# Performance work log

Measured on AMD Instinct MI355X. Metric: run time of the kernel, lower is better.

## Reference

```python
import jax, jax.numpy as jnp
import numpy as np

DT = 0.01
NJ = 7
GRAV = 9.81
Q_LOWER = jnp.array([-2.9671, -1.8326, -2.9671, -3.1416, -2.9671, -0.0873, -2.9671], jnp.float32)
Q_UPPER = jnp.array([ 2.9671,  1.8326,  2.9671,  0.0,     2.9671,  3.8223,  2.9671], jnp.float32)


def _skew(v):
    z = jnp.zeros((), v.dtype)
    return jnp.stack([jnp.stack([z, -v[2], v[1]]),
                      jnp.stack([v[2], z, -v[0]]),
                      jnp.stack([-v[1], v[0], z])])


def _mot_X(E, r):
    # 6x6 spatial motion transform [[E,0],[-E*skew(r),E]]
    zero = jnp.zeros_like(E)
    top = jnp.concatenate([E, zero], axis=1)
    bot = jnp.concatenate([-E @ _skew(r), E], axis=1)
    return jnp.concatenate([top, bot], axis=0)


def _crm(v):
    # spatial motion cross-product matrix for v=[w;v0]
    Sw, Sv = _skew(v[:3]), _skew(v[3:])
    zero = jnp.zeros_like(Sw)
    top = jnp.concatenate([Sw, zero], axis=1)
    bot = jnp.concatenate([Sv, Sw], axis=1)
    return jnp.concatenate([top, bot], axis=0)


def _step_single(x, u, axes, R_tree, p_tree, I_sp):
    dt_ = x.dtype
    q = jnp.clip(x[:NJ], Q_LOWER.astype(dt_), Q_UPPER.astype(dt_))
    qd = x[NJ:]
    # forward kinematics: per-joint 6x6 child<-parent transforms and motion subspaces
    Xups, Ss = [], []
    eye3 = jnp.eye(3, dtype=dt_)
    for i in range(NJ):
        a = axes[i]
        c, s = jnp.cos(q[i]), jnp.sin(q[i])
        R = c * eye3 + s * _skew(a) + (1.0 - c) * jnp.outer(a, a)  # rodrigues
        Xj = _mot_X(R.T, jnp.zeros(3, dt_))
        Xt = _mot_X(R_tree[i], p_tree[i])
        Xups.append(Xj @ Xt)
        Ss.append(jnp.concatenate([a, jnp.zeros(3, dt_)]))
    # RNEA bias force h (qdd=0, gravity, zero base velocity, identity base pose)
    v_prev = jnp.zeros(6, dt_)
    a_prev = jnp.array([0.0, 0.0, 0.0, 0.0, 0.0, GRAV], dt_)  # a_base = -g trick
    fs = []
    for i in range(NJ):
        vJ = Ss[i] * qd[i]
        v = Xups[i] @ v_prev + vJ
        acc = Xups[i] @ a_prev + _crm(v) @ vJ
        Iv = I_sp[i] @ v
        f = I_sp[i] @ acc - _crm(v).T @ Iv  # crf(v) = -crm(v)^T
        fs.append(f)
        v_prev, a_prev = v, acc
    h = [None] * NJ
    for i in range(NJ - 1, -1, -1):
        h[i] = Ss[i] @ fs[i]
        if i > 0:
            fs[i - 1] = fs[i - 1] + Xups[i].T @ fs[i]
    h = jnp.stack(h)
    # CRBA mass matrix (serial chain, parent(i)=i-1)
    Ic = [I_sp[i] for i in range(NJ)]
    M = jnp.zeros((NJ, NJ), dt_)
    for i in range(NJ - 1, -1, -1):
        if i > 0:
            Ic[i - 1] = Ic[i - 1] + Xups[i].T @ Ic[i] @ Xups[i]
        F = Ic[i] @ Ss[i]
        M = M.at[i, i].set(Ss[i] @ F)
        for j in range(i - 1, -1, -1):
            F = Xups[j + 1].T @ F
            mij = Ss[j] @ F
            M = M.at[i, j].set(mij).at[j, i].set(mij)
    M = M + 1e-8 * jnp.eye(NJ, dtype=dt_)
    qdd = jnp.linalg.solve(M, (u - h)[:, None])[:, 0]
    qd_new = qd + DT * qdd
    q_new = q + DT * qd_new
    return jnp.concatenate([q_new, qd_new])


def setup_inputs() -> dict:
    B = 65536
    key = jax.random.key(0)
    k1, k2 = jax.random.split(key)
    x = jax.random.normal(k1, (B, 14), jnp.float32)
    u = jax.random.normal(k2, (B, 7), jnp.float32)
    rng = np.random.default_rng(0)
    # unit joint axes
    axes = rng.normal(size=(NJ, 3))
    axes = axes / np.linalg.norm(axes, axis=1, keepdims=True)
    # orthonormal fixed parent->child rotations (det +1)
    R_tree = np.empty((NJ, 3, 3))
    for i in range(NJ):
        Q, _ = np.linalg.qr(rng.normal(size=(3, 3)))
        if np.linalg.det(Q) < 0:
            Q[:, 0] = -Q[:, 0]
        R_tree[i] = Q
    p_tree = 0.2 * rng.normal(size=(NJ, 3))
    # SPD 6x6 spatial inertias: [[Ibar, m*Cx],[m*Cx^T, m*I3]]
    I_sp = np.empty((NJ, 6, 6))
    for i in range(NJ):
        m = float(rng.uniform(1.0, 5.0))
        c = 0.05 * rng.normal(size=3)
        Cx = np.array([[0, -c[2], c[1]], [c[2], 0, -c[0]], [-c[1], c[0], 0]])
        A = 0.1 * rng.normal(size=(3, 3))
        Ic_ = A @ A.T + 0.05 * np.eye(3)
        Ibar = Ic_ + m * Cx @ Cx.T
        I_sp[i] = np.block([[Ibar, m * Cx], [m * Cx.T, m * np.eye(3)]])
    return {
        "x": x, "u": u,
        "axes": jnp.asarray(axes, jnp.float32),
        "R_tree": jnp.asarray(R_tree, jnp.float32),
        "p_tree": jnp.asarray(p_tree, jnp.float32),
        "I_sp": jnp.asarray(I_sp, jnp.float32),
    }


def reference(x, u, axes, R_tree, p_tree, I_sp):
    return jax.vmap(_step_single, in_axes=(0, 0, None, None, None, None))(
        x, u, axes, R_tree, p_tree, I_sp)
```

## Files before the change

kernel.cpp:

```cpp
#include <hip/hip_runtime.h>
#include <math.h>

#define NJ 7
#define DTF 0.01f
#define GRAVF 9.81f
#define MIX(i,j) ((i)*((i)+1)/2 + (j))
#define MPAD 29
#define FSTR 43
#define SNC  15
#define QST  9

__device__ __forceinline__ void cross3(const float* a, const float* b, float* o){
    o[0] = a[1]*b[2] - a[2]*b[1];
    o[1] = a[2]*b[0] - a[0]*b[2];
    o[2] = a[0]*b[1] - a[1]*b[0];
}
__device__ __forceinline__ void mv3(const float* E, const float* x, float* y){
    y[0] = E[0]*x[0] + E[1]*x[1] + E[2]*x[2];
    y[1] = E[3]*x[0] + E[4]*x[1] + E[5]*x[2];
    y[2] = E[6]*x[0] + E[7]*x[1] + E[8]*x[2];
}
__device__ __forceinline__ void mtv3(const float* E, const float* x, float* y){
    y[0] = E[0]*x[0] + E[3]*x[1] + E[6]*x[2];
    y[1] = E[1]*x[0] + E[4]*x[1] + E[7]*x[2];
    y[2] = E[2]*x[0] + E[5]*x[1] + E[8]*x[2];
}
__device__ __forceinline__ void symv(const float* S, const float* x, float* y){
    y[0] = S[0]*x[0] + S[1]*x[1] + S[2]*x[2];
    y[1] = S[1]*x[0] + S[3]*x[1] + S[4]*x[2];
    y[2] = S[2]*x[0] + S[4]*x[1] + S[5]*x[2];
}
__device__ __forceinline__ void mm3(const float* A, const float* B, float* o){
#pragma unroll
    for (int r = 0; r < 3; r++)
#pragma unroll
        for (int c = 0; c < 3; c++)
            o[r*3+c] = A[r*3]*B[c] + A[r*3+1]*B[3+c] + A[r*3+2]*B[6+c];
}
__device__ __forceinline__ void congr(const float* E, const float* X, float* o){
    float t[9];
#pragma unroll
    for (int r = 0; r < 3; r++)
#pragma unroll
        for (int c = 0; c < 3; c++)
            t[r*3+c] = E[r]*X[c] + E[3+r]*X[3+c] + E[6+r]*X[6+c];
    mm3(t, E, o);
}
__device__ __forceinline__ void makeE(const float* a, const float* __restrict__ Rt,
                                      float s, float c, float* E){
    float omc = 1.0f - c;
    float RT[9];
    RT[0] = c + omc*a[0]*a[0];       RT[1] =  s*a[2] + omc*a[0]*a[1]; RT[2] = -s*a[1] + omc*a[0]*a[2];
    RT[3] = -s*a[2] + omc*a[1]*a[0]; RT[4] = c + omc*a[1]*a[1];       RT[5] =  s*a[0] + omc*a[1]*a[2];
    RT[6] =  s*a[1] + omc*a[2]*a[0]; RT[7] = -s*a[0] + omc*a[2]*a[1]; RT[8] = c + omc*a[2]*a[2];
    float Rl[9];
#pragma unroll
    for (int k = 0; k < 9; k++) Rl[k] = Rt[k];
    mm3(RT, Rl, E);
}
__device__ __forceinline__ void bodyI(const float* __restrict__ g_I, int i,
                                      float* SA, float* h, float& m){
    const float* I6 = g_I + i*36;
    SA[0]=I6[0]; SA[1]=I6[1]; SA[2]=I6[2];
    SA[3]=I6[7]; SA[4]=I6[8]; SA[5]=I6[14];
    h[0]=I6[16]; h[1]=I6[5]; h[2]=I6[9];
    m = I6[21];
}

__constant__ float QL_c[NJ] = {-2.9671f,-1.8326f,-2.9671f,-3.1416f,-2.9671f,-0.0873f,-2.9671f};
__constant__ float QU_c[NJ] = { 2.9671f, 1.8326f, 2.9671f, 0.0f,    2.9671f, 3.8223f, 2.9671f};

__global__ __launch_bounds__(128)
void panda_step(const float* __restrict__ x, const float* __restrict__ u,
                const float* __restrict__ g_ax, const float* __restrict__ g_Rt,
                const float* __restrict__ g_pt, const float* __restrict__ g_I,
                float* __restrict__ out, int B)
{
    __shared__ float s_M[64*MPAD];
    __shared__ float s_F[2*64*FSTR];
    __shared__ float s_snc[64*SNC];
    __shared__ float s_qd[64*QST];
    __shared__ float s_rhs[64*QST];

    const int role = threadIdx.x >> 6;
    const int lane = threadIdx.x & 63;
    const int e    = blockIdx.x*64 + lane;
    const bool act = (e < B);

    float q[NJ], qd[NJ];
    if (act && role == 0){
        float xl[14];
        const float2* x2 = (const float2*)(x + e*14);
#pragma unroll
        for (int i = 0; i < 7; i++){ float2 v = x2[i]; xl[2*i] = v.x; xl[2*i+1] = v.y; }
#pragma unroll
        for (int i = 0; i < NJ; i++){
            q[i]  = fminf(fmaxf(xl[i], QL_c[i]), QU_c[i]);
            qd[i] = xl[NJ + i];
            float s, c; __sincosf(q[i], &s, &c);
            s_snc[lane*SNC + i]     = s;
            s_snc[lane*SNC + 7 + i] = c;
            s_qd[lane*QST + i]      = qd[i];
            s_rhs[lane*QST + i]     = u[e*NJ + i];
        }
    }
    __syncthreads();

    if (act && role == 1){
        float* Fb = &s_F[64*FSTR + lane*FSTR];
        float SA[6], hc[3], mc;
        bodyI(g_I, 6, SA, hc, mc);
#pragma unroll 1
        for (int i = NJ-1; i >= 0; --i){
            float a[3] = { g_ax[3*i], g_ax[3*i+1], g_ax[3*i+2] };
            float p[3] = { g_pt[3*i], g_pt[3*i+1], g_pt[3*i+2] };
            float Ft[3]; symv(SA, a, Ft);
            Fb[i*6+0]=Ft[0]; Fb[i*6+1]=Ft[1]; Fb[i*6+2]=Ft[2];
            Fb[i*6+3] = a[1]*hc[2] - a[2]*hc[1];
            Fb[i*6+4] = a[2]*hc[0] - a[0]*hc[2];
            Fb[i*6+5] = a[0]*hc[1] - a[1]*hc[0];
#pragma unroll 1
            for (int k = i; k < NJ; ++k){
                float f0=Fb[k*6], f1=Fb[k*6+1], f2=Fb[k*6+2];
                s_M[lane*MPAD + k*(k+1)/2 + i] = a[0]*f0 + a[1]*f1 + a[2]*f2;
            }
            if (i > 0){
                float snv = s_snc[lane*SNC+i], csv = s_snc[lane*SNC+7+i];
                float E[9]; makeE(a, g_Rt + 9*i, snv, csv, E);
                float SAm[6], hm[3], mm_;
                bodyI(g_I, i-1, SAm, hm, mm_);
                float Af[9] = {SA[0],SA[1],SA[2], SA[1],SA[3],SA[4], SA[2],SA[4],SA[5]};
                float Ap[9]; congr(E, Af, Ap);
                float hr[3]; mtv3(E, hc, hr);
                float hpd = hr[0]*p[0]+hr[1]*p[1]+hr[2]*p[2];
                float ppd = p[0]*p[0]+p[1]*p[1]+p[2]*p[2];
                float dga = 2.0f*hpd + mc*ppd;
                SA[0] = Ap[0] - 2.0f*p[0]*hr[0] - mc*p[0]*p[0] + dga + SAm[0];
                SA[1] = Ap[1] - p[0]*hr[1] - hr[0]*p[1] - mc*p[0]*p[1] + SAm[1];
                SA[2] = Ap[2] - p[0]*hr[2] - hr[0]*p[2] - mc*p[0]*p[2] + SAm[2];
                SA[3] = Ap[4] - 2.0f*p[1]*hr[1] - mc*p[1]*p[1] + dga + SAm[3];
                SA[4] = Ap[5] - p[1]*hr[2] - hr[1]*p[2] - mc*p[1]*p[2] + SAm[4];
                SA[5] = Ap[8] - 2.0f*p[2]*hr[2] - mc*p[2]*p[2] + dga + SAm[5];
                hc[0] = hr[0] + mc*p[0] + hm[0];
                hc[1] = hr[1] + mc*p[1] + hm[1];
                hc[2] = hr[2] + mc*p[2] + hm[2];
                mc += mm_;
#pragma unroll 1
                for (int k = i; k < NJ; ++k){
                    float ft[3] = {Fb[k*6+0], Fb[k*6+1], Fb[k*6+2]};
                    float fb[3] = {Fb[k*6+3], Fb[k*6+4], Fb[k*6+5]};
                    float tm[3], tf[3], cp[3];
                    mtv3(E, ft, tm); mtv3(E, fb, tf);
                    cross3(p, tf, cp);
                    Fb[k*6+0]=tm[0]+cp[0]; Fb[k*6+1]=tm[1]+cp[1]; Fb[k*6+2]=tm[2]+cp[2];
                    Fb[k*6+3]=tf[0];       Fb[k*6+4]=tf[1];       Fb[k*6+5]=tf[2];
                }
            }
        }
        float Mx[28];
#pragma unroll
        for (int j = 0; j < 28; j++) Mx[j] = s_M[lane*MPAD + j];
#pragma unroll
        for (int i = 0; i < NJ; i++) Mx[MIX(i,i)] += 1e-8f;
#pragma unroll
        for (int k = 0; k < NJ; k++){
            float d = Mx[MIX(k,k)];
#pragma unroll
            for (int j = 0; j < NJ; j++) if (j < k) d -= Mx[MIX(k,j)]*Mx[MIX(k,j)];
            float linv = __builtin_amdgcn_rsqf(d);
            Mx[MIX(k,k)] = linv;
#pragma unroll
            for (int i2 = k+1; i2 < NJ; i2++){
                float s2 = Mx[MIX(i2,k)];
#pragma unroll
                for (int j = 0; j < NJ; j++) if (j < k) s2 -= Mx[MIX(i2,j)]*Mx[MIX(k,j)];
                Mx[MIX(i2,k)] = s2 * linv;
            }
        }
#pragma unroll
        for (int j = 0; j < 28; j++) s_M[lane*MPAD + j] = Mx[j];
    }
    else if (act){
        float* Fb = &s_F[lane*FSTR];
        float w[3]  = {0.f,0.f,0.f}, vl[3] = {0.f,0.f,0.f};
        float aw[3] = {0.f,0.f,0.f}, av[3] = {0.f,0.f,GRAVF};
#pragma unroll 1
        for (int i = 0; i < NJ; ++i){
            float a[3] = { g_ax[3*i], g_ax[3*i+1], g_ax[3*i+2] };
            float p[3] = { g_pt[3*i], g_pt[3*i+1], g_pt[3*i+2] };
            float snv = s_snc[lane*SNC+i], csv = s_snc[lane*SNC+7+i];
            float qdi = s_qd[lane*QST+i];
            float E[9]; makeE(a, g_Rt + 9*i, snv, csv, E);
            float tw[3]; mv3(E, w, tw);
            float nw[3] = { tw[0]+a[0]*qdi, tw[1]+a[1]*qdi, tw[2]+a[2]*qdi };
            float cwp[3]; cross3(w, p, cwp);
            float t1[3] = { vl[0]+cwp[0], vl[1]+cwp[1], vl[2]+cwp[2] };
            float nvl[3]; mv3(E, t1, nvl);
            float taw[3]; mv3(E, aw, taw);
            float cna[3]; cross3(nw, a, cna);
            float naw[3] = { taw[0]+qdi*cna[0], taw[1]+qdi*cna[1], taw[2]+qdi*cna[2] };
            float cap[3]; cross3(aw, p, cap);
            float t2[3] = { av[0]+cap[0], av[1]+cap[1], av[2]+cap[2] };
            float tav[3]; mv3(E, t2, tav);
            float cva[3]; cross3(nvl, a, cva);
            float nav[3] = { tav[0]+qdi*cva[0], tav[1]+qdi*cva[1], tav[2]+qdi*cva[2] };
            float SAi[6], hi[3], mi; bodyI(g_I, i, SAi, hi, mi);
            float Ivt[3], Iat[3], hxv[3], hxa[3];
            symv(SAi, nw, Ivt);  cross3(hi, nvl, hxv);
            symv(SAi, naw, Iat); cross3(hi, nav, hxa);
#pragma unroll
            for (int k = 0; k < 3; k++){ Ivt[k] += hxv[k]; Iat[k] += hxa[k]; }
            float hxw[3], hxaw[3];
            cross3(hi, nw, hxw); cross3(hi, naw, hxaw);
            float Ivb[3] = { mi*nvl[0]-hxw[0], mi*nvl[1]-hxw[1], mi*nvl[2]-hxw[2] };
            float Iab[3] = { mi*nav[0]-hxaw[0], mi*nav[1]-hxaw[1], mi*nav[2]-hxaw[2] };
            float c1[3], c2[3], c3[3];
            cross3(nw, Ivt, c1); cross3(nvl, Ivb, c2); cross3(nw, Ivb, c3);
            Fb[i*6+0] = Iat[0]+c1[0]+c2[0];
            Fb[i*6+1] = Iat[1]+c1[1]+c2[1];
            Fb[i*6+2] = Iat[2]+c1[2]+c2[2];
            Fb[i*6+3] = Iab[0]+c3[0];
            Fb[i*6+4] = Iab[1]+c3[1];
            Fb[i*6+5] = Iab[2]+c3[2];
#pragma unroll
            for (int k = 0; k < 3; k++){ w[k]=nw[k]; vl[k]=nvl[k]; aw[k]=naw[k]; av[k]=nav[k]; }
        }
#pragma unroll 1
        for (int i = NJ-1; i >= 0; --i){
            float a[3] = { g_ax[3*i], g_ax[3*i+1], g_ax[3*i+2] };
            float f0=Fb[i*6+0], f1=Fb[i*6+1], f2=Fb[i*6+2];
            s_rhs[lane*QST+i] -= a[0]*f0 + a[1]*f1 + a[2]*f2;
            if (i > 0){
                float p[3] = { g_pt[3*i], g_pt[3*i+1], g_pt[3*i+2] };
                float snv = s_snc[lane*SNC+i], csv = s_snc[lane*SNC+7+i];
                float E[9]; makeE(a, g_Rt + 9*i, snv, csv, E);
                float ftop[3] = {f0, f1, f2};
                float fbot[3] = {Fb[i*6+3], Fb[i*6+4], Fb[i*6+5]};
                float tm[3], tf[3], cp[3];
                mtv3(E, ftop, tm); mtv3(E, fbot, tf);
                cross3(p, tf, cp);
                Fb[(i-1)*6+0] += tm[0]+cp[0];
                Fb[(i-1)*6+1] += tm[1]+cp[1];
                Fb[(i-1)*6+2] += tm[2]+cp[2];
                Fb[(i-1)*6+3] += tf[0];
                Fb[(i-1)*6+4] += tf[1];
                Fb[(i-1)*6+5] += tf[2];
            }
        }
    }

    __syncthreads();

    if (act && role == 0){
        float Mx[28];
#pragma unroll
        for (int j = 0; j < 28; j++) Mx[j] = s_M[lane*MPAD + j];
        float rhs[NJ];
#pragma unroll
        for (int i = 0; i < NJ; i++) rhs[i] = s_rhs[lane*QST + i];
        float y[NJ];
#pragma unroll
        for (int i = 0; i < NJ; i++){
            float s2 = rhs[i];
#pragma unroll
            for (int j = 0; j < NJ; j++) if (j < i) s2 -= Mx[MIX(i,j)]*y[j];
            y[i] = s2 * Mx[MIX(i,i)];
        }
        float z[NJ];
#pragma unroll
        for (int i = NJ-1; i >= 0; i--){
            float s2 = y[i];
#pragma unroll
            for (int j = NJ-1; j >= 0; j--) if (j > i) s2 -= Mx[MIX(j,i)]*z[j];
            z[i] = s2 * Mx[MIX(i,i)];
        }
        float o14[14];
#pragma unroll
        for (int i = 0; i < NJ; i++){
            float qdn = qd[i] + DTF*z[i];
            o14[i]      = q[i] + DTF*qdn;
            o14[NJ + i] = qdn;
        }
        float2* o2 = (float2*)(out + e*14);
#pragma unroll
        for (int i = 0; i < 7; i++){ float2 v; v.x = o14[2*i]; v.y = o14[2*i+1]; o2[i] = v; }
    }
}

extern "C" void kernel_launch(void* const* d_in, const int* in_sizes, int n_in,
                              void* d_out, int out_size, void* d_ws, size_t ws_size,
                              hipStream_t stream) {
    const float* x   = (const float*)d_in[0];
    const float* u   = (const float*)d_in[1];
    const float* ax  = (const float*)d_in[2];
    const float* Rt  = (const float*)d_in[3];
    const float* pt  = (const float*)d_in[4];
    const float* Isp = (const float*)d_in[5];
    float* out = (float*)d_out;
    int B = in_sizes[0] / 14;
    int grid = (B + 63) / 64;
    hipLaunchKernelGGL(panda_step, dim3(grid), dim3(128), 0, stream,
                       x, u, ax, Rt, pt, Isp, out, B);
}
```

Measured before the change: 78.58 us.

## Keep per-joint spatial forces and mass matrix in registers, fully unroll joint loops

```diff
diff --git a/kernel.cpp b/kernel.cpp
--- a/kernel.cpp
+++ b/kernel.cpp
@@ -5,8 +5,6 @@
 #define DTF 0.01f
 #define GRAVF 9.81f
 #define MIX(i,j) ((i)*((i)+1)/2 + (j))
-#define MPAD 29
-#define FSTR 43
 #define SNC  15
 #define QST  9
 
@@ -70,16 +68,15 @@
 __constant__ float QL_c[NJ] = {-2.9671f,-1.8326f,-2.9671f,-3.1416f,-2.9671f,-0.0873f,-2.9671f};
 __constant__ float QU_c[NJ] = { 2.9671f, 1.8326f, 2.9671f, 0.0f,    2.9671f, 3.8223f, 2.9671f};
 
-__global__ __launch_bounds__(128)
+__global__ __launch_bounds__(128, 2)
 void panda_step(const float* __restrict__ x, const float* __restrict__ u,
                 const float* __restrict__ g_ax, const float* __restrict__ g_Rt,
                 const float* __restrict__ g_pt, const float* __restrict__ g_I,
                 float* __restrict__ out, int B)
 {
-    __shared__ float s_M[64*MPAD];
-    __shared__ float s_F[2*64*FSTR];
     __shared__ float s_snc[64*SNC];
-    __shared__ float s_qd[64*QST];
+    __shared__ float s_q  [64*QST];
+    __shared__ float s_qd [64*QST];
     __shared__ float s_rhs[64*QST];
 
     const int role = threadIdx.x >> 6;
@@ -87,46 +84,56 @@
     const int e    = blockIdx.x*64 + lane;
     const bool act = (e < B);
 
-    float q[NJ], qd[NJ];
+    float a_all[3*NJ], p_all[3*NJ];
+#pragma unroll
+    for (int j = 0; j < 3*NJ; j++){ a_all[j] = g_ax[j]; p_all[j] = g_pt[j]; }
+    float SA[6], hc[3], mc;
+    bodyI(g_I, 6, SA, hc, mc);
+
+    float q[NJ], qd[NJ], sn[NJ], cs[NJ], uu[NJ];
     if (act && role == 0){
+        const float2* x2 = (const float2*)(x + e*14);
         float xl[14];
-        const float2* x2 = (const float2*)(x + e*14);
 #pragma unroll
         for (int i = 0; i < 7; i++){ float2 v = x2[i]; xl[2*i] = v.x; xl[2*i+1] = v.y; }
 #pragma unroll
         for (int i = 0; i < NJ; i++){
             q[i]  = fminf(fmaxf(xl[i], QL_c[i]), QU_c[i]);
             qd[i] = xl[NJ + i];
-            float s, c; __sincosf(q[i], &s, &c);
-            s_snc[lane*SNC + i]     = s;
-            s_snc[lane*SNC + 7 + i] = c;
+            uu[i] = u[e*NJ + i];
+            __sincosf(q[i], &sn[i], &cs[i]);
+            s_snc[lane*SNC + i]     = sn[i];
+            s_snc[lane*SNC + 7 + i] = cs[i];
+            s_q [lane*QST + i]      = q[i];
             s_qd[lane*QST + i]      = qd[i];
-            s_rhs[lane*QST + i]     = u[e*NJ + i];
         }
     }
     __syncthreads();
 
-    if (act && role == 1){
-        float* Fb = &s_F[64*FSTR + lane*FSTR];
-        float SA[6], hc[3], mc;
-        bodyI(g_I, 6, SA, hc, mc);
-#pragma unroll 1
+    float Mx[28];
+    if (act){
+      if (role == 1){
+        float sn1[NJ], cs1[NJ];
+#pragma unroll
+        for (int i = 0; i < NJ; i++){
+            sn1[i] = s_snc[lane*SNC + i];
+            cs1[i] = s_snc[lane*SNC + 7 + i];
+        }
+        float Fb[6*NJ];
+#pragma unroll
         for (int i = NJ-1; i >= 0; --i){
-            float a[3] = { g_ax[3*i], g_ax[3*i+1], g_ax[3*i+2] };
-            float p[3] = { g_pt[3*i], g_pt[3*i+1], g_pt[3*i+2] };
+            float a[3] = { a_all[3*i], a_all[3*i+1], a_all[3*i+2] };
             float Ft[3]; symv(SA, a, Ft);
             Fb[i*6+0]=Ft[0]; Fb[i*6+1]=Ft[1]; Fb[i*6+2]=Ft[2];
             Fb[i*6+3] = a[1]*hc[2] - a[2]*hc[1];
             Fb[i*6+4] = a[2]*hc[0] - a[0]*hc[2];
             Fb[i*6+5] = a[0]*hc[1] - a[1]*hc[0];
-#pragma unroll 1
-            for (int k = i; k < NJ; ++k){
-                float f0=Fb[k*6], f1=Fb[k*6+1], f2=Fb[k*6+2];
-                s_M[lane*MPAD + k*(k+1)/2 + i] = a[0]*f0 + a[1]*f1 + a[2]*f2;
-            }
+#pragma unroll
+            for (int k = i; k < NJ; ++k)
+                Mx[MIX(k,i)] = a[0]*Fb[k*6] + a[1]*Fb[k*6+1] + a[2]*Fb[k*6+2];
             if (i > 0){
-                float snv = s_snc[lane*SNC+i], csv = s_snc[lane*SNC+7+i];
-                float E[9]; makeE(a, g_Rt + 9*i, snv, csv, E);
+                float p[3] = { p_all[3*i], p_all[3*i+1], p_all[3*i+2] };
+                float E[9]; makeE(a, g_Rt + 9*i, sn1[i], cs1[i], E);
                 float SAm[6], hm[3], mm_;
                 bodyI(g_I, i-1, SAm, hm, mm_);
                 float Af[9] = {SA[0],SA[1],SA[2], SA[1],SA[3],SA[4], SA[2],SA[4],SA[5]};
@@ -145,21 +152,18 @@
                 hc[1] = hr[1] + mc*p[1] + hm[1];
                 hc[2] = hr[2] + mc*p[2] + hm[2];
                 mc += mm_;
-#pragma unroll 1
+#pragma unroll
                 for (int k = i; k < NJ; ++k){
                     float ft[3] = {Fb[k*6+0], Fb[k*6+1], Fb[k*6+2]};
-                    float fb[3] = {Fb[k*6+3], Fb[k*6+4], Fb[k*6+5]};
+                    float fb2[3] = {Fb[k*6+3], Fb[k*6+4], Fb[k*6+5]};
                     float tm[3], tf[3], cp[3];
-                    mtv3(E, ft, tm); mtv3(E, fb, tf);
+                    mtv3(E, ft, tm); mtv3(E, fb2, tf);
                     cross3(p, tf, cp);
                     Fb[k*6+0]=tm[0]+cp[0]; Fb[k*6+1]=tm[1]+cp[1]; Fb[k*6+2]=tm[2]+cp[2];
                     Fb[k*6+3]=tf[0];       Fb[k*6+4]=tf[1];       Fb[k*6+5]=tf[2];
                 }
             }
         }
-        float Mx[28];
-#pragma unroll
-        for (int j = 0; j < 28; j++) Mx[j] = s_M[lane*MPAD + j];
 #pragma unroll
         for (int i = 0; i < NJ; i++) Mx[MIX(i,i)] += 1e-8f;
 #pragma unroll
@@ -177,20 +181,16 @@
                 Mx[MIX(i2,k)] = s2 * linv;
             }
         }
-#pragma unroll
-        for (int j = 0; j < 28; j++) s_M[lane*MPAD + j] = Mx[j];
-    }
-    else if (act){
-        float* Fb = &s_F[lane*FSTR];
+      } else {
+        float Fb[6*NJ];
         float w[3]  = {0.f,0.f,0.f}, vl[3] = {0.f,0.f,0.f};
-        float aw[3] = {0.f,0.f,0.f}, av[3] = {0.f,0.f,GRAVF};
-#pragma unroll 1
+        float aw[3] = {0.f,0.f,0.f}, avv[3] = {0.f,0.f,GRAVF};
+#pragma unroll
         for (int i = 0; i < NJ; ++i){
-            float a[3] = { g_ax[3*i], g_ax[3*i+1], g_ax[3*i+2] };
-            float p[3] = { g_pt[3*i], g_pt[3*i+1], g_pt[3*i+2] };
-            float snv = s_snc[lane*SNC+i], csv = s_snc[lane*SNC+7+i];
-            float qdi = s_qd[lane*QST+i];
-            float E[9]; makeE(a, g_Rt + 9*i, snv, csv, E);
+            float a[3] = { a_all[3*i], a_all[3*i+1], a_all[3*i+2] };
+            float p[3] = { p_all[3*i], p_all[3*i+1], p_all[3*i+2] };
+            float qdi = qd[i];
+            float E[9]; makeE(a, g_Rt + 9*i, sn[i], cs[i], E);
             float tw[3]; mv3(E, w, tw);
             float nw[3] = { tw[0]+a[0]*qdi, tw[1]+a[1]*qdi, tw[2]+a[2]*qdi };
             float cwp[3]; cross3(w, p, cwp);
@@ -200,7 +200,7 @@
             float cna[3]; cross3(nw, a, cna);
             float naw[3] = { taw[0]+qdi*cna[0], taw[1]+qdi*cna[1], taw[2]+qdi*cna[2] };
             float cap[3]; cross3(aw, p, cap);
-            float t2[3] = { av[0]+cap[0], av[1]+cap[1], av[2]+cap[2] };
+            float t2[3] = { avv[0]+cap[0], avv[1]+cap[1], avv[2]+cap[2] };
             float tav[3]; mv3(E, t2, tav);
             float cva[3]; cross3(nvl, a, cva);
             float nav[3] = { tav[0]+qdi*cva[0], tav[1]+qdi*cva[1], tav[2]+qdi*cva[2] };
@@ -223,17 +223,16 @@
             Fb[i*6+4] = Iab[1]+c3[1];
             Fb[i*6+5] = Iab[2]+c3[2];
 #pragma unroll
-            for (int k = 0; k < 3; k++){ w[k]=nw[k]; vl[k]=nvl[k]; aw[k]=naw[k]; av[k]=nav[k]; }
-        }
-#pragma unroll 1
+            for (int k = 0; k < 3; k++){ w[k]=nw[k]; vl[k]=nvl[k]; aw[k]=naw[k]; avv[k]=nav[k]; }
+        }
+#pragma unroll
         for (int i = NJ-1; i >= 0; --i){
-            float a[3] = { g_ax[3*i], g_ax[3*i+1], g_ax[3*i+2] };
+            float a[3] = { a_all[3*i], a_all[3*i+1], a_all[3*i+2] };
             float f0=Fb[i*6+0], f1=Fb[i*6+1], f2=Fb[i*6+2];
-            s_rhs[lane*QST+i] -= a[0]*f0 + a[1]*f1 + a[2]*f2;
+            s_rhs[lane*QST + i] = uu[i] - (a[0]*f0 + a[1]*f1 + a[2]*f2);
             if (i > 0){
-                float p[3] = { g_pt[3*i], g_pt[3*i+1], g_pt[3*i+2] };
-                float snv = s_snc[lane*SNC+i], csv = s_snc[lane*SNC+7+i];
-                float E[9]; makeE(a, g_Rt + 9*i, snv, csv, E);
+                float p[3] = { p_all[3*i], p_all[3*i+1], p_all[3*i+2] };
+                float E[9]; makeE(a, g_Rt + 9*i, sn[i], cs[i], E);
                 float ftop[3] = {f0, f1, f2};
                 float fbot[3] = {Fb[i*6+3], Fb[i*6+4], Fb[i*6+5]};
                 float tm[3], tf[3], cp[3];
@@ -247,14 +246,12 @@
                 Fb[(i-1)*6+5] += tf[2];
             }
         }
+      }
     }
 
     __syncthreads();
 
-    if (act && role == 0){
-        float Mx[28];
-#pragma unroll
-        for (int j = 0; j < 28; j++) Mx[j] = s_M[lane*MPAD + j];
+    if (act && role == 1){
         float rhs[NJ];
 #pragma unroll
         for (int i = 0; i < NJ; i++) rhs[i] = s_rhs[lane*QST + i];
@@ -277,8 +274,10 @@
         float o14[14];
 #pragma unroll
         for (int i = 0; i < NJ; i++){
-            float qdn = qd[i] + DTF*z[i];
-            o14[i]      = q[i] + DTF*qdn;
+            float qv  = s_q [lane*QST + i];
+            float qdv = s_qd[lane*QST + i];
+            float qdn = qdv + DTF*z[i];
+            o14[i]      = qv + DTF*qdn;
             o14[NJ + i] = qdn;
         }
         float2* o2 = (float2*)(out + e*14);
```

After: 83.13 us. +5.8%, slower.

## Remove first barrier, fuse CRBA mass-matrix writes into force transform loop

Applied to the files above, without the earlier changes.

```diff
diff --git a/kernel.cpp b/kernel.cpp
--- a/kernel.cpp
+++ b/kernel.cpp
@@ -5,10 +5,10 @@
 #define DTF 0.01f
 #define GRAVF 9.81f
 #define MIX(i,j) ((i)*((i)+1)/2 + (j))
-#define MPAD 29
 #define FSTR 43
 #define SNC  15
-#define QST  9
+#define MRST 35
+#define QDS  7
 
 __device__ __forceinline__ void cross3(const float* a, const float* b, float* o){
     o[0] = a[1]*b[2] - a[2]*b[1];
@@ -70,25 +70,25 @@
 __constant__ float QL_c[NJ] = {-2.9671f,-1.8326f,-2.9671f,-3.1416f,-2.9671f,-0.0873f,-2.9671f};
 __constant__ float QU_c[NJ] = { 2.9671f, 1.8326f, 2.9671f, 0.0f,    2.9671f, 3.8223f, 2.9671f};
 
-__global__ __launch_bounds__(128)
+__global__ __launch_bounds__(128, 2)
 void panda_step(const float* __restrict__ x, const float* __restrict__ u,
                 const float* __restrict__ g_ax, const float* __restrict__ g_Rt,
                 const float* __restrict__ g_pt, const float* __restrict__ g_I,
                 float* __restrict__ out, int B)
 {
-    __shared__ float s_M[64*MPAD];
-    __shared__ float s_F[2*64*FSTR];
-    __shared__ float s_snc[64*SNC];
-    __shared__ float s_qd[64*QST];
-    __shared__ float s_rhs[64*QST];
+    __shared__ float s_Mr [64*MRST];
+    __shared__ float s_F  [2*64*FSTR];
+    __shared__ float s_snc[2*64*SNC];
+    __shared__ float s_qd [64*QDS];
 
     const int role = threadIdx.x >> 6;
     const int lane = threadIdx.x & 63;
     const int e    = blockIdx.x*64 + lane;
     const bool act = (e < B);
+    const int sncb = (role*64 + lane)*SNC;
 
     float q[NJ], qd[NJ];
-    if (act && role == 0){
+    if (act){
         float xl[14];
         const float2* x2 = (const float2*)(x + e*14);
 #pragma unroll
@@ -98,34 +98,36 @@
             q[i]  = fminf(fmaxf(xl[i], QL_c[i]), QU_c[i]);
             qd[i] = xl[NJ + i];
             float s, c; __sincosf(q[i], &s, &c);
-            s_snc[lane*SNC + i]     = s;
-            s_snc[lane*SNC + 7 + i] = c;
-            s_qd[lane*QST + i]      = qd[i];
-            s_rhs[lane*QST + i]     = u[e*NJ + i];
+            s_snc[sncb + i]     = s;
+            s_snc[sncb + 7 + i] = c;
+        }
+        if (role == 0){
+#pragma unroll
+            for (int i = 0; i < NJ; i++){
+                s_qd [lane*QDS + i]       = qd[i];
+                s_Mr [lane*MRST + 28 + i] = u[e*NJ + i];
+            }
         }
     }
-    __syncthreads();
 
     if (act && role == 1){
-        float* Fb = &s_F[64*FSTR + lane*FSTR];
+        float* Fb = &s_F[(64 + lane)*FSTR];
         float SA[6], hc[3], mc;
         bodyI(g_I, 6, SA, hc, mc);
 #pragma unroll 1
         for (int i = NJ-1; i >= 0; --i){
             float a[3] = { g_ax[3*i], g_ax[3*i+1], g_ax[3*i+2] };
-            float p[3] = { g_pt[3*i], g_pt[3*i+1], g_pt[3*i+2] };
             float Ft[3]; symv(SA, a, Ft);
+            float Fbt[3];
+            Fbt[0] = a[1]*hc[2] - a[2]*hc[1];
+            Fbt[1] = a[2]*hc[0] - a[0]*hc[2];
+            Fbt[2] = a[0]*hc[1] - a[1]*hc[0];
+            s_Mr[lane*MRST + (i*(i+3)>>1)] = a[0]*Ft[0] + a[1]*Ft[1] + a[2]*Ft[2];
             Fb[i*6+0]=Ft[0]; Fb[i*6+1]=Ft[1]; Fb[i*6+2]=Ft[2];
-            Fb[i*6+3] = a[1]*hc[2] - a[2]*hc[1];
-            Fb[i*6+4] = a[2]*hc[0] - a[0]*hc[2];
-            Fb[i*6+5] = a[0]*hc[1] - a[1]*hc[0];
-#pragma unroll 1
-            for (int k = i; k < NJ; ++k){
-                float f0=Fb[k*6], f1=Fb[k*6+1], f2=Fb[k*6+2];
-                s_M[lane*MPAD + k*(k+1)/2 + i] = a[0]*f0 + a[1]*f1 + a[2]*f2;
-            }
+            Fb[i*6+3]=Fbt[0]; Fb[i*6+4]=Fbt[1]; Fb[i*6+5]=Fbt[2];
             if (i > 0){
-                float snv = s_snc[lane*SNC+i], csv = s_snc[lane*SNC+7+i];
+                float p[3] = { g_pt[3*i], g_pt[3*i+1], g_pt[3*i+2] };
+                float snv = s_snc[sncb + i], csv = s_snc[sncb + 7 + i];
                 float E[9]; makeE(a, g_Rt + 9*i, snv, csv, E);
                 float SAm[6], hm[3], mm_;
                 bodyI(g_I, i-1, SAm, hm, mm_);
@@ -145,21 +147,27 @@
                 hc[1] = hr[1] + mc*p[1] + hm[1];
                 hc[2] = hr[2] + mc*p[2] + hm[2];
                 mc += mm_;
-#pragma unroll 1
-                for (int k = i; k < NJ; ++k){
-                    float ft[3] = {Fb[k*6+0], Fb[k*6+1], Fb[k*6+2]};
-                    float fb[3] = {Fb[k*6+3], Fb[k*6+4], Fb[k*6+5]};
-                    float tm[3], tf[3], cp[3];
-                    mtv3(E, ft, tm); mtv3(E, fb, tf);
-                    cross3(p, tf, cp);
-                    Fb[k*6+0]=tm[0]+cp[0]; Fb[k*6+1]=tm[1]+cp[1]; Fb[k*6+2]=tm[2]+cp[2];
-                    Fb[k*6+3]=tf[0];       Fb[k*6+4]=tf[1];       Fb[k*6+5]=tf[2];
+                float an[3] = { g_ax[3*(i-1)], g_ax[3*(i-1)+1], g_ax[3*(i-1)+2] };
+#pragma unroll
+                for (int k = 0; k < NJ; ++k){
+                    if (k >= i){
+                        float ft[3]  = {Fb[k*6+0], Fb[k*6+1], Fb[k*6+2]};
+                        float fb2[3] = {Fb[k*6+3], Fb[k*6+4], Fb[k*6+5]};
+                        float tm[3], tf[3], cp[3];
+                        mtv3(E, ft, tm); mtv3(E, fb2, tf);
+                        cross3(p, tf, cp);
+                        float n0 = tm[0]+cp[0], n1 = tm[1]+cp[1], n2 = tm[2]+cp[2];
+                        Fb[k*6+0]=n0; Fb[k*6+1]=n1; Fb[k*6+2]=n2;
+                        Fb[k*6+3]=tf[0]; Fb[k*6+4]=tf[1]; Fb[k*6+5]=tf[2];
+                        s_Mr[lane*MRST + (k*(k+1)/2) + (i-1)] =
+                            an[0]*n0 + an[1]*n1 + an[2]*n2;
+                    }
                 }
             }
         }
         float Mx[28];
 #pragma unroll
-        for (int j = 0; j < 28; j++) Mx[j] = s_M[lane*MPAD + j];
+        for (int j = 0; j < 28; j++) Mx[j] = s_Mr[lane*MRST + j];
 #pragma unroll
         for (int i = 0; i < NJ; i++) Mx[MIX(i,i)] += 1e-8f;
 #pragma unroll
@@ -178,7 +186,7 @@
             }
         }
 #pragma unroll
-        for (int j = 0; j < 28; j++) s_M[lane*MPAD + j] = Mx[j];
+        for (int j = 0; j < 28; j++) s_Mr[lane*MRST + j] = Mx[j];
     }
     else if (act){
         float* Fb = &s_F[lane*FSTR];
@@ -188,8 +196,8 @@
         for (int i = 0; i < NJ; ++i){
             float a[3] = { g_ax[3*i], g_ax[3*i+1], g_ax[3*i+2] };
             float p[3] = { g_pt[3*i], g_pt[3*i+1], g_pt[3*i+2] };
-            float snv = s_snc[lane*SNC+i], csv = s_snc[lane*SNC+7+i];
-            float qdi = s_qd[lane*QST+i];
+            float snv = s_snc[sncb + i], csv = s_snc[sncb + 7 + i];
+            float qdi = s_qd[lane*QDS + i];
             float E[9]; makeE(a, g_Rt + 9*i, snv, csv, E);
             float tw[3]; mv3(E, w, tw);
             float nw[3] = { tw[0]+a[0]*qdi, tw[1]+a[1]*qdi, tw[2]+a[2]*qdi };
@@ -225,27 +233,31 @@
 #pragma unroll
             for (int k = 0; k < 3; k++){ w[k]=nw[k]; vl[k]=nvl[k]; aw[k]=naw[k]; av[k]=nav[k]; }
         }
+        float f[6];
+#pragma unroll
+        for (int k = 0; k < 6; k++) f[k] = Fb[36 + k];
 #pragma unroll 1
-        for (int i = NJ-1; i >= 0; --i){
+        for (int i = NJ-1; i >= 1; --i){
             float a[3] = { g_ax[3*i], g_ax[3*i+1], g_ax[3*i+2] };
-            float f0=Fb[i*6+0], f1=Fb[i*6+1], f2=Fb[i*6+2];
-            s_rhs[lane*QST+i] -= a[0]*f0 + a[1]*f1 + a[2]*f2;
-            if (i > 0){
-                float p[3] = { g_pt[3*i], g_pt[3*i+1], g_pt[3*i+2] };
-                float snv = s_snc[lane*SNC+i], csv = s_snc[lane*SNC+7+i];
-                float E[9]; makeE(a, g_Rt + 9*i, snv, csv, E);
-                float ftop[3] = {f0, f1, f2};
-                float fbot[3] = {Fb[i*6+3], Fb[i*6+4], Fb[i*6+5]};
-                float tm[3], tf[3], cp[3];
-                mtv3(E, ftop, tm); mtv3(E, fbot, tf);
-                cross3(p, tf, cp);
-                Fb[(i-1)*6+0] += tm[0]+cp[0];
-                Fb[(i-1)*6+1] += tm[1]+cp[1];
-                Fb[(i-1)*6+2] += tm[2]+cp[2];
-                Fb[(i-1)*6+3] += tf[0];
-                Fb[(i-1)*6+4] += tf[1];
-                Fb[(i-1)*6+5] += tf[2];
-            }
+            s_Mr[lane*MRST + 28 + i] -= a[0]*f[0] + a[1]*f[1] + a[2]*f[2];
+            float p[3] = { g_pt[3*i], g_pt[3*i+1], g_pt[3*i+2] };
+            float snv = s_snc[sncb + i], csv = s_snc[sncb + 7 + i];
+            float E[9]; makeE(a, g_Rt + 9*i, snv, csv, E);
+            float ftop[3] = {f[0], f[1], f[2]};
+            float fbot[3] = {f[3], f[4], f[5]};
+            float tm[3], tf[3], cp[3];
+            mtv3(E, ftop, tm); mtv3(E, fbot, tf);
+            cross3(p, tf, cp);
+            f[0] = Fb[(i-1)*6+0] + tm[0]+cp[0];
+            f[1] = Fb[(i-1)*6+1] + tm[1]+cp[1];
+            f[2] = Fb[(i-1)*6+2] + tm[2]+cp[2];
+            f[3] = Fb[(i-1)*6+3] + tf[0];
+            f[4] = Fb[(i-1)*6+4] + tf[1];
+            f[5] = Fb[(i-1)*6+5] + tf[2];
+        }
+        {
+            float a0[3] = { g_ax[0], g_ax[1], g_ax[2] };
+            s_Mr[lane*MRST + 28] -= a0[0]*f[0] + a0[1]*f[1] + a0[2]*f[2];
         }
     }
 
@@ -254,10 +266,10 @@
     if (act && role == 0){
         float Mx[28];
 #pragma unroll
-        for (int j = 0; j < 28; j++) Mx[j] = s_M[lane*MPAD + j];
+        for (int j = 0; j < 28; j++) Mx[j] = s_Mr[lane*MRST + j];
         float rhs[NJ];
 #pragma unroll
-        for (int i = 0; i < NJ; i++) rhs[i] = s_rhs[lane*QST + i];
+        for (int i = 0; i < NJ; i++) rhs[i] = s_Mr[lane*MRST + 28 + i];
         float y[NJ];
 #pragma unroll
         for (int i = 0; i < NJ; i++){
```

Result: no change. 77.05 us (median of 2 runs) (-1.9%).
